# Kernel tuning notes

Measured on AMD Instinct MI355X. Metric: run time of the kernel, lower is better.

## Reference

```python
import jax, jax.numpy as jnp
import numpy as np
import math

B, T, D = 4, 8192, 1024
EPS = 1e-5

def setup_inputs() -> dict:
    key = jax.random.key(0)
    ks = jax.random.split(key, 8)
    xavier = lambda k, shape: jax.random.uniform(k, shape, jnp.float32,
                                                 -math.sqrt(6.0 / (shape[0] + shape[1])),
                                                 math.sqrt(6.0 / (shape[0] + shape[1])))
    x = jax.random.normal(ks[0], (B, T, D), jnp.float32)
    ln_gamma = jnp.ones((D,), jnp.float32)
    ln_beta = jnp.zeros((D,), jnp.float32)
    Wg = xavier(ks[1], (D, D))            # torch Linear weight: (out, in)
    bg = jnp.zeros((D,), jnp.float32)
    Wv = 0.01 * xavier(ks[2], (D, D))     # gain=0.01
    bv = jnp.zeros((D,), jnp.float32)
    Wo = 0.01 * xavier(ks[3], (D, D))     # gain=0.01
    bo = jnp.zeros((D,), jnp.float32)
    log_decay = jnp.asarray(math.log(math.exp(0.01) - 1.0), jnp.float32)
    return {"x": x, "ln_gamma": ln_gamma, "ln_beta": ln_beta,
            "Wg": Wg, "bg": bg, "Wv": Wv, "bv": bv, "Wo": Wo, "bo": bo,
            "log_decay": log_decay}

def reference(x, ln_gamma, ln_beta, Wg, bg, Wv, bv, Wo, bo, log_decay):
    # LayerNorm
    mu = jnp.mean(x, axis=-1, keepdims=True)
    var = jnp.mean(jnp.square(x - mu), axis=-1, keepdims=True)
    normed = (x - mu) * jax.lax.rsqrt(var + EPS) * ln_gamma + ln_beta
    # gate / value projections (torch Linear: y = x @ W.T + b)
    g = jax.nn.sigmoid(jnp.einsum('btd,ed->bte', normed, Wg) + bg)
    v = jnp.einsum('btd,ed->bte', normed, Wv) + bv
    # push-pull cumulative sums over time
    cumsum = jnp.cumsum(g * v, axis=1) - jnp.cumsum((1.0 - g) * v, axis=1)
    # positional exponential decay
    alpha = jax.nn.softplus(log_decay)
    positions = jnp.arange(x.shape[1], dtype=jnp.float32)
    decay = jnp.exp(-alpha * positions)[None, :, None]  # (1,T,1)
    out = jnp.einsum('btd,ed->bte', cumsum * decay, Wo) + bo
    return x + out  # dropout is identity at eval
```

## Files before the change

kernel.cpp:

```cpp
#include <hip/hip_runtime.h>
#include <cstdint>
#include <cstddef>

#define DD 1024
#define TT 8192
#define BB 4
#define MM (BB*TT)
#define NCHUNK 64
#define CLEN 128
#define EPS 1e-5f
#define NK2 16

typedef __attribute__((ext_vector_type(8))) short bf16x8;
typedef __attribute__((ext_vector_type(4))) float f32x4;

__device__ __forceinline__ float bf2f(unsigned short b) {
  union { unsigned int u; float f; } c; c.u = ((unsigned int)b) << 16; return c.f;
}
__device__ __forceinline__ unsigned short f2bf(float f) {
  union { float f; unsigned int u; } c; c.f = f;
  unsigned int lsb = (c.u >> 16) & 1u;
  c.u += 0x7fffu + lsb;
  return (unsigned short)(c.u >> 16);
}

__device__ __forceinline__ void gload16(const void* gsrc, void* ldst) {
  __builtin_amdgcn_global_load_lds(
      (const __attribute__((address_space(1))) unsigned int*)gsrc,
      (__attribute__((address_space(3))) unsigned int*)ldst, 16, 0, 0);
}

#define SWZ(row) (((row) >> 1) & 3)

template<int R>
__device__ __forceinline__ void stageT(const unsigned short* __restrict__ g,
                                       size_t row0, int k0,
                                       unsigned short* lds, int tid) {
#pragma unroll
  for (int l = 0; l < R / 128; ++l) {
    int u16 = l * 512 + tid;
    int row = u16 >> 2;
    int sp  = u16 & 3;
    int sl  = sp ^ SWZ(row);
    const unsigned short* src = g + (row0 + (size_t)row) * DD + k0 + sl * 8;
    gload16(src, (char*)lds + (size_t)u16 * 16);
  }
}

__device__ __forceinline__ bf16x8 ldsfrag(const unsigned short* lds, int row, int sl) {
  int sp = sl ^ SWZ(row);
  return *(const bf16x8*)&lds[row * 32 + sp * 8];
}

#define MFMA16(a, b, c) __builtin_amdgcn_mfma_f32_16x16x32_bf16((a), (b), (c), 0, 0, 0)

__device__ __forceinline__ void lgkm0_fence() {
  asm volatile("s_waitcnt lgkmcnt(0)" ::: "memory");
  __builtin_amdgcn_sched_barrier(0);
}

__global__ __launch_bounds__(256) void cast_weights(
    const float* __restrict__ wg, const float* __restrict__ wv,
    const float* __restrict__ wo,
    unsigned short* __restrict__ owg, unsigned short* __restrict__ owv,
    unsigned short* __restrict__ owo) {
  int i = blockIdx.x * 256 + threadIdx.x;
  const float* src; unsigned short* dst; int off;
  if (i < 262144)       { src = wg; dst = owg; off = i; }
  else if (i < 524288)  { src = wv; dst = owv; off = i - 262144; }
  else                  { src = wo; dst = owo; off = i - 524288; }
  float4 v = ((const float4*)src)[off];
  ushort4 o;
  o.x = f2bf(v.x); o.y = f2bf(v.y); o.z = f2bf(v.z); o.w = f2bf(v.w);
  ((ushort4*)dst)[off] = o;
}

__global__ __launch_bounds__(256) void ln_kernel(
    const float* __restrict__ x, const float* __restrict__ gamma,
    const float* __restrict__ beta, unsigned short* __restrict__ normed) {
  size_t row = blockIdx.x;
  int tid = threadIdx.x, lane = tid & 63, wid = tid >> 6;
  float4 v = ((const float4*)(x + row * DD))[tid];
  float s = v.x + v.y + v.z + v.w;
  float q = v.x * v.x + v.y * v.y + v.z * v.z + v.w * v.w;
#pragma unroll
  for (int off = 32; off; off >>= 1) {
    s += __shfl_down(s, off);
    q += __shfl_down(q, off);
  }
  __shared__ float rs[4], rq[4];
  if (lane == 0) { rs[wid] = s; rq[wid] = q; }
  __syncthreads();
  float ts = rs[0] + rs[1] + rs[2] + rs[3];
  float tq = rq[0] + rq[1] + rq[2] + rq[3];
  float mu  = ts * (1.0f / DD);
  float var = tq * (1.0f / DD) - mu * mu;
  float rstd = rsqrtf(var + EPS);
  float4 gm = ((const float4*)gamma)[tid];
  float4 bt = ((const float4*)beta)[tid];
  ushort4 o;
  o.x = f2bf((v.x - mu) * rstd * gm.x + bt.x);
  o.y = f2bf((v.y - mu) * rstd * gm.y + bt.y);
  o.z = f2bf((v.z - mu) * rstd * gm.z + bt.z);
  o.w = f2bf((v.w - mu) * rstd * gm.w + bt.w);
  ((ushort4*)normed)[row * (DD / 4) + tid] = o;
}

__global__ __launch_bounds__(512, 2) void gemm_gv(
    const unsigned short* __restrict__ normed,
    const unsigned short* __restrict__ wg, const unsigned short* __restrict__ wv,
    const float* __restrict__ bg, const float* __restrict__ bv,
    unsigned short* __restrict__ u, float* __restrict__ sums) {
  __shared__ unsigned short As[2][2][256 * 32];
  __shared__ unsigned short Bgs[2][2][128 * 32];
  __shared__ unsigned short Bvs[2][2][128 * 32];
  int tid = threadIdx.x, lane = tid & 63, wid = tid >> 6;
  int wm = wid >> 2, wn = wid & 3;
  int nwg = gridDim.x;
  int swz = (blockIdx.x & 7) * (nwg >> 3) + (blockIdx.x >> 3);
  int bx = swz >> 3;
  int by = swz & 7;
  size_t m0 = (size_t)bx * 256;
  int n0 = by * 128;

  f32x4 accg[8][2], accv[8][2];
#pragma unroll
  for (int a = 0; a < 8; ++a)
#pragma unroll
    for (int b = 0; b < 2; ++b) {
      accg[a][b] = (f32x4){0.f, 0.f, 0.f, 0.f};
      accv[a][b] = (f32x4){0.f, 0.f, 0.f, 0.f};
    }

  stageT<256>(normed, m0, 0,  As[0][0], tid);
  stageT<128>(wg, (size_t)n0, 0,  Bgs[0][0], tid);
  stageT<128>(wv, (size_t)n0, 0,  Bvs[0][0], tid);
  stageT<256>(normed, m0, 32, As[0][1], tid);
  stageT<128>(wg, (size_t)n0, 32, Bgs[0][1], tid);
  stageT<128>(wv, (size_t)n0, 32, Bvs[0][1], tid);
  asm volatile("s_waitcnt vmcnt(4)" ::: "memory");
  __builtin_amdgcn_s_barrier();

  int r = lane & 15, q = lane >> 4;
  for (int t = 0; t < NK2; ++t) {
    int buf = t & 1;
    int k1 = (t + 1) * 64;
    bool more = (t + 1 < NK2);
    bf16x8 af[8], b0, b1;
#pragma unroll
    for (int mi = 0; mi < 8; ++mi)
      af[mi] = ldsfrag(As[buf][0], wm * 128 + mi * 16 + r, q);
    b0 = ldsfrag(Bgs[buf][0], wn * 32 + r, q);
    b1 = ldsfrag(Bgs[buf][0], wn * 32 + 16 + r, q);
    if (more) stageT<256>(normed, m0, k1, As[buf ^ 1][0], tid);
    __builtin_amdgcn_s_barrier();
    lgkm0_fence();
    __builtin_amdgcn_s_setprio(1);
#pragma unroll
    for (int mi = 0; mi < 8; ++mi) {
      accg[mi][0] = MFMA16(af[mi], b0, accg[mi][0]);
      accg[mi][1] = MFMA16(af[mi], b1, accg[mi][1]);
    }
    __builtin_amdgcn_s_setprio(0);
    __builtin_amdgcn_s_barrier();
    b0 = ldsfrag(Bvs[buf][0], wn * 32 + r, q);
    b1 = ldsfrag(Bvs[buf][0], wn * 32 + 16 + r, q);
    if (more) {
      stageT<128>(wg, (size_t)n0, k1, Bgs[buf ^ 1][0], tid);
      stageT<128>(wv, (size_t)n0, k1, Bvs[buf ^ 1][0], tid);
    }
    __builtin_amdgcn_s_barrier();
    lgkm0_fence();
    __builtin_amdgcn_s_setprio(1);
#pragma unroll
    for (int mi = 0; mi < 8; ++mi) {
      accv[mi][0] = MFMA16(af[mi], b0, accv[mi][0]);
      accv[mi][1] = MFMA16(af[mi], b1, accv[mi][1]);
    }
    __builtin_amdgcn_s_setprio(0);
    if (more) asm volatile("s_waitcnt vmcnt(4)" ::: "memory");
    else      asm volatile("s_waitcnt vmcnt(0)" ::: "memory");
    __builtin_amdgcn_s_barrier();
#pragma unroll
    for (int mi = 0; mi < 8; ++mi)
      af[mi] = ldsfrag(As[buf][1], wm * 128 + mi * 16 + r, q);
    b0 = ldsfrag(Bvs[buf][1], wn * 32 + r, q);
    b1 = ldsfrag(Bvs[buf][1], wn * 32 + 16 + r, q);
    if (more) stageT<256>(normed, m0, k1 + 32, As[buf ^ 1][1], tid);
    __builtin_amdgcn_s_barrier();
    lgkm0_fence();
    __builtin_amdgcn_s_setprio(1);
#pragma unroll
    for (int mi = 0; mi < 8; ++mi) {
      accv[mi][0] = MFMA16(af[mi], b0, accv[mi][0]);
      accv[mi][1] = MFMA16(af[mi], b1, accv[mi][1]);
    }
    __builtin_amdgcn_s_setprio(0);
    __builtin_amdgcn_s_barrier();
    b0 = ldsfrag(Bgs[buf][1], wn * 32 + r, q);
    b1 = ldsfrag(Bgs[buf][1], wn * 32 + 16 + r, q);
    if (more) {
      stageT<128>(wg, (size_t)n0, k1 + 32, Bgs[buf ^ 1][1], tid);
      stageT<128>(wv, (size_t)n0, k1 + 32, Bvs[buf ^ 1][1], tid);
    }
    __builtin_amdgcn_s_barrier();
    lgkm0_fence();
    __builtin_amdgcn_s_setprio(1);
#pragma unroll
    for (int mi = 0; mi < 8; ++mi) {
      accg[mi][0] = MFMA16(af[mi], b0, accg[mi][0]);
      accg[mi][1] = MFMA16(af[mi], b1, accg[mi][1]);
    }
    __builtin_amdgcn_s_setprio(0);
    if (more) asm volatile("s_waitcnt vmcnt(4)" ::: "memory");
    __builtin_amdgcn_s_barrier();
  }

  float psum[2] = {0.f, 0.f};
#pragma unroll
  for (int mi = 0; mi < 8; ++mi)
#pragma unroll
    for (int ni = 0; ni < 2; ++ni) {
      int e = n0 + wn * 32 + ni * 16 + r;
      size_t rbase = m0 + wm * 128 + mi * 16 + q * 4;
      float bgv = bg[e], bvv = bv[e];
#pragma unroll
      for (int j = 0; j < 4; ++j) {
        float gp = accg[mi][ni][j] + bgv;
        float vp = accv[mi][ni][j] + bvv;
        float sg = 1.0f / (1.0f + __expf(-gp));
        float uu = (2.0f * sg - 1.0f) * vp;
        psum[ni] += uu;
        u[(rbase + j) * DD + e] = f2bf(uu);
      }
    }
#pragma unroll
  for (int ni = 0; ni < 2; ++ni) {
    psum[ni] += __shfl_xor(psum[ni], 16);
    psum[ni] += __shfl_xor(psum[ni], 32);
  }
  if (lane < 16) {
    int b = (int)(m0 >> 13);
    int ch = (int)((m0 & 8191) >> 7) + wm;
    size_t sidx = ((size_t)(b * NCHUNK + ch)) * DD + n0 + wn * 32 + lane;
    sums[sidx]      = psum[0];
    sums[sidx + 16] = psum[1];
  }
}

__global__ __launch_bounds__(256) void scan_chunks(float* __restrict__ sums) {
  int b = blockIdx.x >> 2;
  int e = (blockIdx.x & 3) * 256 + threadIdx.x;
  float vals[NCHUNK];
#pragma unroll
  for (int c = 0; c < NCHUNK; ++c)
    vals[c] = sums[((size_t)(b * NCHUNK + c)) * DD + e];
  float carry = 0.f;
#pragma unroll
  for (int c = 0; c < NCHUNK; ++c) {
    float t = vals[c]; vals[c] = carry; carry += t;
  }
#pragma unroll
  for (int c = 0; c < NCHUNK; ++c)
    sums[((size_t)(b * NCHUNK + c)) * DD + e] = vals[c];
}

__global__ __launch_bounds__(128) void scan_final(
    unsigned short* __restrict__ u, const float* __restrict__ sums,
    const float* __restrict__ log_decay) {
  int bid = blockIdx.x;
  int half = bid & 1, chunk = (bid >> 1) & 63, b = bid >> 7;
  int e0 = half * 512 + threadIdx.x * 4;
  float alpha = log1pf(__expf(log_decay[0]));
  float4 c = *(const float4*)(sums + ((size_t)(b * NCHUNK + chunk)) * DD + e0);
  size_t base = ((size_t)b * TT + (size_t)chunk * CLEN) * DD + e0;
#pragma unroll 4
  for (int i = 0; i < CLEN; ++i) {
    int t = chunk * CLEN + i;
    float dec = __expf(-alpha * (float)t);
    ushort4 w = *(const ushort4*)(u + base + (size_t)i * DD);
    c.x += bf2f(w.x); c.y += bf2f(w.y); c.z += bf2f(w.z); c.w += bf2f(w.w);
    ushort4 o;
    o.x = f2bf(c.x * dec); o.y = f2bf(c.y * dec);
    o.z = f2bf(c.z * dec); o.w = f2bf(c.w * dec);
    *(ushort4*)(u + base + (size_t)i * DD) = o;
  }
}

__global__ __launch_bounds__(512, 2) void gemm_out(
    const unsigned short* __restrict__ cmat, const unsigned short* __restrict__ wo,
    const float* __restrict__ bo, const float* __restrict__ x,
    float* __restrict__ out) {
  __shared__ unsigned short As[2][2][256 * 32];
  __shared__ unsigned short Bs[2][2][256 * 32];
  int tid = threadIdx.x, lane = tid & 63, wid = tid >> 6;
  int wm = wid >> 2, wn = wid & 3;
  int nwg = gridDim.x;
  int swz = (blockIdx.x & 7) * (nwg >> 3) + (blockIdx.x >> 3);
  int bx = swz >> 2;
  int by = swz & 3;
  size_t m0 = (size_t)bx * 256;
  int n0 = by * 256;

  f32x4 acc[8][4];
#pragma unroll
  for (int a = 0; a < 8; ++a)
#pragma unroll
    for (int b = 0; b < 4; ++b) acc[a][b] = (f32x4){0.f, 0.f, 0.f, 0.f};

  stageT<256>(cmat, m0, 0,  As[0][0], tid);
  stageT<256>(wo, (size_t)n0, 0,  Bs[0][0], tid);
  stageT<256>(cmat, m0, 32, As[0][1], tid);
  stageT<256>(wo, (size_t)n0, 32, Bs[0][1], tid);
  asm volatile("s_waitcnt vmcnt(4)" ::: "memory");
  __builtin_amdgcn_s_barrier();

  int r = lane & 15, q = lane >> 4;
  for (int t = 0; t < NK2; ++t) {
    int buf = t & 1;
    int k1 = (t + 1) * 64;
    bool more = (t + 1 < NK2);
    bf16x8 af[8], b0, b1;
#pragma unroll
    for (int mi = 0; mi < 8; ++mi)
      af[mi] = ldsfrag(As[buf][0], wm * 128 + mi * 16 + r, q);
    b0 = ldsfrag(Bs[buf][0], wn * 64 + r, q);
    b1 = ldsfrag(Bs[buf][0], wn * 64 + 16 + r, q);
    if (more) stageT<256>(cmat, m0, k1, As[buf ^ 1][0], tid);
    __builtin_amdgcn_s_barrier();
    lgkm0_fence();
    __builtin_amdgcn_s_setprio(1);
#pragma unroll
    for (int mi = 0; mi < 8; ++mi) {
      acc[mi][0] = MFMA16(af[mi], b0, acc[mi][0]);
      acc[mi][1] = MFMA16(af[mi], b1, acc[mi][1]);
    }
    __builtin_amdgcn_s_setprio(0);
    __builtin_amdgcn_s_barrier();
    b0 = ldsfrag(Bs[buf][0], wn * 64 + 32 + r, q);
    b1 = ldsfrag(Bs[buf][0], wn * 64 + 48 + r, q);
    if (more) stageT<256>(wo, (size_t)n0, k1, Bs[buf ^ 1][0], tid);
    __builtin_amdgcn_s_barrier();
    lgkm0_fence();
    __builtin_amdgcn_s_setprio(1);
#pragma unroll
    for (int mi = 0; mi < 8; ++mi) {
      acc[mi][2] = MFMA16(af[mi], b0, acc[mi][2]);
      acc[mi][3] = MFMA16(af[mi], b1, acc[mi][3]);
    }
    __builtin_amdgcn_s_setprio(0);
    if (more) asm volatile("s_waitcnt vmcnt(4)" ::: "memory");
    else      asm volatile("s_waitcnt vmcnt(0)" ::: "memory");
    __builtin_amdgcn_s_barrier();
#pragma unroll
    for (int mi = 0; mi < 8; ++mi)
      af[mi] = ldsfrag(As[buf][1], wm * 128 + mi * 16 + r, q);
    b0 = ldsfrag(Bs[buf][1], wn * 64 + 32 + r, q);
    b1 = ldsfrag(Bs[buf][1], wn * 64 + 48 + r, q);
    if (more) stageT<256>(cmat, m0, k1 + 32, As[buf ^ 1][1], tid);
    __builtin_amdgcn_s_barrier();
    lgkm0_fence();
    __builtin_amdgcn_s_setprio(1);
#pragma unroll
    for (int mi = 0; mi < 8; ++mi) {
      acc[mi][2] = MFMA16(af[mi], b0, acc[mi][2]);
      acc[mi][3] = MFMA16(af[mi], b1, acc[mi][3]);
    }
    __builtin_amdgcn_s_setprio(0);
    __builtin_amdgcn_s_barrier();
    b0 = ldsfrag(Bs[buf][1], wn * 64 + r, q);
    b1 = ldsfrag(Bs[buf][1], wn * 64 + 16 + r, q);
    if (more) stageT<256>(wo, (size_t)n0, k1 + 32, Bs[buf ^ 1][1], tid);
    __builtin_amdgcn_s_barrier();
    lgkm0_fence();
    __builtin_amdgcn_s_setprio(1);
#pragma unroll
    for (int mi = 0; mi < 8; ++mi) {
      acc[mi][0] = MFMA16(af[mi], b0, acc[mi][0]);
      acc[mi][1] = MFMA16(af[mi], b1, acc[mi][1]);
    }
    __builtin_amdgcn_s_setprio(0);
    if (more) asm volatile("s_waitcnt vmcnt(4)" ::: "memory");
    __builtin_amdgcn_s_barrier();
  }

#pragma unroll
  for (int mi = 0; mi < 8; ++mi)
#pragma unroll
    for (int nq = 0; nq < 4; ++nq) {
      int e = n0 + wn * 64 + nq * 16 + r;
      size_t rbase = m0 + wm * 128 + mi * 16 + q * 4;
      float bov = bo[e];
#pragma unroll
      for (int j = 0; j < 4; ++j) {
        size_t idx = (rbase + j) * DD + e;
        out[idx] = x[idx] + bov + acc[mi][nq][j];
      }
    }
}

extern "C" void kernel_launch(void* const* d_in, const int* in_sizes, int n_in,
                              void* d_out, int out_size, void* d_ws, size_t ws_size,
                              hipStream_t stream) {
  const float* x     = (const float*)d_in[0];
  const float* gamma = (const float*)d_in[1];
  const float* beta  = (const float*)d_in[2];
  const float* Wg    = (const float*)d_in[3];
  const float* bg    = (const float*)d_in[4];
  const float* Wv    = (const float*)d_in[5];
  const float* bv    = (const float*)d_in[6];
  const float* Wo    = (const float*)d_in[7];
  const float* bo    = (const float*)d_in[8];
  const float* ldcy  = (const float*)d_in[9];
  float* out = (float*)d_out;

  char* ws = (char*)d_ws;
  unsigned short* normed = (unsigned short*)ws;
  unsigned short* u      = (unsigned short*)(ws + (size_t)67108864);
  unsigned short* wgb    = (unsigned short*)(ws + (size_t)134217728);
  unsigned short* wvb    = wgb + 1048576;
  unsigned short* wob    = wvb + 1048576;
  float* sums            = (float*)(ws + (size_t)134217728 + (size_t)3 * 2097152);

  cast_weights<<<3072, 256, 0, stream>>>(Wg, Wv, Wo, wgb, wvb, wob);
  ln_kernel<<<MM, 256, 0, stream>>>(x, gamma, beta, normed);
  gemm_gv<<<dim3(MM / 256 * (DD / 128)), 512, 0, stream>>>(normed, wgb, wvb, bg, bv, u, sums);
  scan_chunks<<<BB * (DD / 256), 256, 0, stream>>>(sums);
  scan_final<<<BB * NCHUNK * 2, 128, 0, stream>>>(u, sums, ldcy);
  gemm_out<<<dim3(MM / 256 * (DD / 256)), 512, 0, stream>>>(u, wob, bo, x, out);
}
```

Measured before the change: 328.3 us.

## Deepen GEMM prefetch to three half-stages and cut per-iteration barriers

Restructures the software pipeline in both MFMA GEMM kernels. Each K half-stage (A and B tiles) is now issued as one unit, three half-stages ahead, and the wait uses vmcnt(8) with one barrier per half-iteration. This replaces the previous pattern of several s_barrier and lgkmcnt(0) fences per half, which stalled MFMA issue. The aim is more latency hiding for global-to-LDS loads and fewer workgroup synchronisations. The trade-off is more outstanding loads in flight and a tighter LDS reuse window, which risks a race if reads of a buffer have not retired before it is overwritten.

```diff
diff --git a/kernel.cpp b/kernel.cpp
--- a/kernel.cpp
+++ b/kernel.cpp
@@ -54,8 +54,13 @@
 
 #define MFMA16(a, b, c) __builtin_amdgcn_mfma_f32_16x16x32_bf16((a), (b), (c), 0, 0, 0)
 
-__device__ __forceinline__ void lgkm0_fence() {
-  asm volatile("s_waitcnt lgkmcnt(0)" ::: "memory");
+template<int N>
+__device__ __forceinline__ void half_sync() {
+  __builtin_amdgcn_sched_barrier(0);
+  if constexpr (N == 8)      asm volatile("s_waitcnt vmcnt(8)" ::: "memory");
+  else if constexpr (N == 4) asm volatile("s_waitcnt vmcnt(4)" ::: "memory");
+  else                       asm volatile("s_waitcnt vmcnt(0)" ::: "memory");
+  __builtin_amdgcn_s_barrier();
   __builtin_amdgcn_sched_barrier(0);
 }
 
@@ -132,29 +137,26 @@
       accv[a][b] = (f32x4){0.f, 0.f, 0.f, 0.f};
     }
 
-  stageT<256>(normed, m0, 0,  As[0][0], tid);
-  stageT<128>(wg, (size_t)n0, 0,  Bgs[0][0], tid);
-  stageT<128>(wv, (size_t)n0, 0,  Bvs[0][0], tid);
-  stageT<256>(normed, m0, 32, As[0][1], tid);
-  stageT<128>(wg, (size_t)n0, 32, Bgs[0][1], tid);
-  stageT<128>(wv, (size_t)n0, 32, Bvs[0][1], tid);
-  asm volatile("s_waitcnt vmcnt(4)" ::: "memory");
-  __builtin_amdgcn_s_barrier();
+  auto STAGE = [&](int h) {
+    int t = h >> 1, kh = h & 1, k0 = t * 64 + kh * 32;
+    stageT<256>(normed, m0, k0, As[t & 1][kh], tid);
+    stageT<128>(wg, (size_t)n0, k0, Bgs[t & 1][kh], tid);
+    stageT<128>(wv, (size_t)n0, k0, Bvs[t & 1][kh], tid);
+  };
+
+  STAGE(0); STAGE(1); STAGE(2);
+  half_sync<8>();
 
   int r = lane & 15, q = lane >> 4;
+  bf16x8 af[8], b0, b1;
   for (int t = 0; t < NK2; ++t) {
     int buf = t & 1;
-    int k1 = (t + 1) * 64;
-    bool more = (t + 1 < NK2);
-    bf16x8 af[8], b0, b1;
 #pragma unroll
     for (int mi = 0; mi < 8; ++mi)
       af[mi] = ldsfrag(As[buf][0], wm * 128 + mi * 16 + r, q);
     b0 = ldsfrag(Bgs[buf][0], wn * 32 + r, q);
     b1 = ldsfrag(Bgs[buf][0], wn * 32 + 16 + r, q);
-    if (more) stageT<256>(normed, m0, k1, As[buf ^ 1][0], tid);
-    __builtin_amdgcn_s_barrier();
-    lgkm0_fence();
+    if (t < NK2 - 1) STAGE(2 * t + 3);
     __builtin_amdgcn_s_setprio(1);
 #pragma unroll
     for (int mi = 0; mi < 8; ++mi) {
@@ -162,15 +164,8 @@
       accg[mi][1] = MFMA16(af[mi], b1, accg[mi][1]);
     }
     __builtin_amdgcn_s_setprio(0);
-    __builtin_amdgcn_s_barrier();
     b0 = ldsfrag(Bvs[buf][0], wn * 32 + r, q);
     b1 = ldsfrag(Bvs[buf][0], wn * 32 + 16 + r, q);
-    if (more) {
-      stageT<128>(wg, (size_t)n0, k1, Bgs[buf ^ 1][0], tid);
-      stageT<128>(wv, (size_t)n0, k1, Bvs[buf ^ 1][0], tid);
-    }
-    __builtin_amdgcn_s_barrier();
-    lgkm0_fence();
     __builtin_amdgcn_s_setprio(1);
 #pragma unroll
     for (int mi = 0; mi < 8; ++mi) {
@@ -178,17 +173,14 @@
       accv[mi][1] = MFMA16(af[mi], b1, accv[mi][1]);
     }
     __builtin_amdgcn_s_setprio(0);
-    if (more) asm volatile("s_waitcnt vmcnt(4)" ::: "memory");
-    else      asm volatile("s_waitcnt vmcnt(0)" ::: "memory");
-    __builtin_amdgcn_s_barrier();
+    if (t < NK2 - 1) half_sync<8>();
+    else             half_sync<0>();
 #pragma unroll
     for (int mi = 0; mi < 8; ++mi)
       af[mi] = ldsfrag(As[buf][1], wm * 128 + mi * 16 + r, q);
     b0 = ldsfrag(Bvs[buf][1], wn * 32 + r, q);
     b1 = ldsfrag(Bvs[buf][1], wn * 32 + 16 + r, q);
-    if (more) stageT<256>(normed, m0, k1 + 32, As[buf ^ 1][1], tid);
-    __builtin_amdgcn_s_barrier();
-    lgkm0_fence();
+    if (t < NK2 - 2) STAGE(2 * t + 4);
     __builtin_amdgcn_s_setprio(1);
 #pragma unroll
     for (int mi = 0; mi < 8; ++mi) {
@@ -196,15 +188,8 @@
       accv[mi][1] = MFMA16(af[mi], b1, accv[mi][1]);
     }
     __builtin_amdgcn_s_setprio(0);
-    __builtin_amdgcn_s_barrier();
     b0 = ldsfrag(Bgs[buf][1], wn * 32 + r, q);
     b1 = ldsfrag(Bgs[buf][1], wn * 32 + 16 + r, q);
-    if (more) {
-      stageT<128>(wg, (size_t)n0, k1 + 32, Bgs[buf ^ 1][1], tid);
-      stageT<128>(wv, (size_t)n0, k1 + 32, Bvs[buf ^ 1][1], tid);
-    }
-    __builtin_amdgcn_s_barrier();
-    lgkm0_fence();
     __builtin_amdgcn_s_setprio(1);
 #pragma unroll
     for (int mi = 0; mi < 8; ++mi) {
@@ -212,8 +197,8 @@
       accg[mi][1] = MFMA16(af[mi], b1, accg[mi][1]);
     }
     __builtin_amdgcn_s_setprio(0);
-    if (more) asm volatile("s_waitcnt vmcnt(4)" ::: "memory");
-    __builtin_amdgcn_s_barrier();
+    if (t < NK2 - 2)      half_sync<8>();
+    else if (t == NK2 - 2) half_sync<4>();
   }
 
   float psum[2] = {0.f, 0.f};
@@ -308,27 +293,25 @@
 #pragma unroll
     for (int b = 0; b < 4; ++b) acc[a][b] = (f32x4){0.f, 0.f, 0.f, 0.f};
 
-  stageT<256>(cmat, m0, 0,  As[0][0], tid);
-  stageT<256>(wo, (size_t)n0, 0,  Bs[0][0], tid);
-  stageT<256>(cmat, m0, 32, As[0][1], tid);
-  stageT<256>(wo, (size_t)n0, 32, Bs[0][1], tid);
-  asm volatile("s_waitcnt vmcnt(4)" ::: "memory");
-  __builtin_amdgcn_s_barrier();
+  auto STAGE = [&](int h) {
+    int t = h >> 1, kh = h & 1, k0 = t * 64 + kh * 32;
+    stageT<256>(cmat, m0, k0, As[t & 1][kh], tid);
+    stageT<256>(wo, (size_t)n0, k0, Bs[t & 1][kh], tid);
+  };
+
+  STAGE(0); STAGE(1); STAGE(2);
+  half_sync<8>();
 
   int r = lane & 15, q = lane >> 4;
+  bf16x8 af[8], b0, b1;
   for (int t = 0; t < NK2; ++t) {
     int buf = t & 1;
-    int k1 = (t + 1) * 64;
-    bool more = (t + 1 < NK2);
-    bf16x8 af[8], b0, b1;
 #pragma unroll
     for (int mi = 0; mi < 8; ++mi)
       af[mi] = ldsfrag(As[buf][0], wm * 128 + mi * 16 + r, q);
     b0 = ldsfrag(Bs[buf][0], wn * 64 + r, q);
     b1 = ldsfrag(Bs[buf][0], wn * 64 + 16 + r, q);
-    if (more) stageT<256>(cmat, m0, k1, As[buf ^ 1][0], tid);
-    __builtin_amdgcn_s_barrier();
-    lgkm0_fence();
+    if (t < NK2 - 1) STAGE(2 * t + 3);
     __builtin_amdgcn_s_setprio(1);
 #pragma unroll
     for (int mi = 0; mi < 8; ++mi) {
@@ -336,12 +319,8 @@
       acc[mi][1] = MFMA16(af[mi], b1, acc[mi][1]);
     }
     __builtin_amdgcn_s_setprio(0);
-    __builtin_amdgcn_s_barrier();
     b0 = ldsfrag(Bs[buf][0], wn * 64 + 32 + r, q);
     b1 = ldsfrag(Bs[buf][0], wn * 64 + 48 + r, q);
-    if (more) stageT<256>(wo, (size_t)n0, k1, Bs[buf ^ 1][0], tid);
-    __builtin_amdgcn_s_barrier();
-    lgkm0_fence();
     __builtin_amdgcn_s_setprio(1);
 #pragma unroll
     for (int mi = 0; mi < 8; ++mi) {
@@ -349,17 +328,23 @@
       acc[mi][3] = MFMA16(af[mi], b1, acc[mi][3]);
     }
     __builtin_amdgcn_s_setprio(0);
-    if (more) asm volatile("s_waitcnt vmcnt(4)" ::: "memory");
-    else      asm volatile("s_waitcnt vmcnt(0)" ::: "memory");
-    __builtin_amdgcn_s_barrier();
+    if (t < NK2 - 1) half_sync<8>();
+    else             half_sync<0>();
 #pragma unroll
     for (int mi = 0; mi < 8; ++mi)
       af[mi] = ldsfrag(As[buf][1], wm * 128 + mi * 16 + r, q);
+    b0 = ldsfrag(Bs[buf][1], wn * 64 + r, q);
+    b1 = ldsfrag(Bs[buf][1], wn * 64 + 16 + r, q);
+    if (t < NK2 - 2) STAGE(2 * t + 4);
+    __builtin_amdgcn_s_setprio(1);
+#pragma unroll
+    for (int mi = 0; mi < 8; ++mi) {
+      acc[mi][0] = MFMA16(af[mi], b0, acc[mi][0]);
+      acc[mi][1] = MFMA16(af[mi], b1, acc[mi][1]);
+    }
+    __builtin_amdgcn_s_setprio(0);
     b0 = ldsfrag(Bs[buf][1], wn * 64 + 32 + r, q);
     b1 = ldsfrag(Bs[buf][1], wn * 64 + 48 + r, q);
-    if (more) stageT<256>(cmat, m0, k1 + 32, As[buf ^ 1][1], tid);
-    __builtin_amdgcn_s_barrier();
-    lgkm0_fence();
     __builtin_amdgcn_s_setprio(1);
 #pragma unroll
     for (int mi = 0; mi < 8; ++mi) {
@@ -367,21 +352,8 @@
       acc[mi][3] = MFMA16(af[mi], b1, acc[mi][3]);
     }
     __builtin_amdgcn_s_setprio(0);
-    __builtin_amdgcn_s_barrier();
-    b0 = ldsfrag(Bs[buf][1], wn * 64 + r, q);
-    b1 = ldsfrag(Bs[buf][1], wn * 64 + 16 + r, q);
-    if (more) stageT<256>(wo, (size_t)n0, k1 + 32, Bs[buf ^ 1][1], tid);
-    __builtin_amdgcn_s_barrier();
-    lgkm0_fence();
-    __builtin_amdgcn_s_setprio(1);
-#pragma unroll
-    for (int mi = 0; mi < 8; ++mi) {
-      acc[mi][0] = MFMA16(af[mi], b0, acc[mi][0]);
-      acc[mi][1] = MFMA16(af[mi], b1, acc[mi][1]);
-    }
-    __builtin_amdgcn_s_setprio(0);
-    if (more) asm volatile("s_waitcnt vmcnt(4)" ::: "memory");
-    __builtin_amdgcn_s_barrier();
+    if (t < NK2 - 2)       half_sync<8>();
+    else if (t == NK2 - 2) half_sync<4>();
   }
 
 #pragma unroll
```

Measured after the change: 337.0 us. 1.03x slower.
